# Kernel optimization log

Measured on AMD Instinct MI355X. Metric: run time of the kernel, lower is better.

Reference implementation:

```python
import jax, jax.numpy as jnp
import numpy as np

B, C, H, W = 16, 64, 64, 64
K = 512  # n_embeddings


def setup_inputs() -> dict:
    key = jax.random.key(0)
    k1, k2 = jax.random.split(key)
    inputs = jax.random.normal(k1, (B, C, H, W), dtype=jnp.float32)
    emb_weight = jax.random.normal(k2, (K, C), dtype=jnp.float32)
    weight = jnp.ones((K,), dtype=jnp.float32)  # EMA cluster-size buffer
    return {"inputs": inputs, "emb_weight": emb_weight, "weight": weight}


def reference(inputs, emb_weight, weight):
    sg = jax.lax.stop_gradient
    # BCHW -> BHWC
    x = jnp.transpose(inputs, (0, 2, 3, 1))  # [B,H,W,C]
    flat = x.reshape(-1, x.shape[-1])        # [N,C]
    n = flat.shape[0]
    k = emb_weight.shape[0]
    # squared euclidean distances [N,K] (argmin identical to cdist argmin)
    d = (
        jnp.sum(flat * flat, axis=-1, keepdims=True)
        - 2.0 * (flat @ emb_weight.T)
        + jnp.sum(emb_weight * emb_weight, axis=-1)
    )
    indices = jnp.argmin(d, axis=1)  # [N]
    # avg_probs = mean over rows of one-hot mask == normalized histogram
    avg_probs = jnp.bincount(indices, length=k).astype(jnp.float32) / jnp.float32(n)
    perplexity = jnp.exp(-jnp.sum(avg_probs * jnp.log(avg_probs + 1e-10)))
    # straight-through quantization
    q = emb_weight[indices].reshape(x.shape)  # [B,H,W,C]
    quantized = sg(q) + x - sg(x)
    commitment_loss = jnp.mean((sg(quantized) - x) ** 2)
    active_codes = jnp.sum(weight >= 0.01)
    out = jnp.transpose(quantized, (0, 3, 1, 2))  # back to BCHW
    return out, commitment_loss, perplexity, active_codes, indices
```

## Files before the change

kernel.cpp:

```cpp
#include <hip/hip_runtime.h>

#define HW 4096
#define CHW 262144
#define OUT_ELEMS 4194304
#define FLT_BIG 3.4e38f

typedef __attribute__((ext_vector_type(8))) short  short8;
typedef __attribute__((ext_vector_type(4))) float  floatx4;
typedef __attribute__((ext_vector_type(4))) int    intx4;


__device__ __forceinline__ unsigned bf16_rne(float f) {
    unsigned u = __float_as_uint(f);
    return (u + 0x7FFFu + ((u >> 16) & 1u)) >> 16;
}

__device__ __forceinline__ void split8(const float* f, intx4* hi, intx4* lo) {
    unsigned h[4], l[4];
#pragma unroll
    for (int j = 0; j < 4; ++j) {
        const unsigned h0 = bf16_rne(f[2 * j]);
        const unsigned h1 = bf16_rne(f[2 * j + 1]);
        const float hf0 = __uint_as_float(h0 << 16);
        const float hf1 = __uint_as_float(h1 << 16);
        const unsigned l0 = bf16_rne(f[2 * j] - hf0);
        const unsigned l1 = bf16_rne(f[2 * j + 1] - hf1);
        h[j] = h0 | (h1 << 16);
        l[j] = l0 | (l1 << 16);
    }
    *hi = intx4{(int)h[0], (int)h[1], (int)h[2], (int)h[3]};
    *lo = intx4{(int)l[0], (int)l[1], (int)l[2], (int)l[3]};
}

__global__ void vq_prep(const float* __restrict__ emb,
                        unsigned short* __restrict__ pfrag,
                        float* __restrict__ enorm) {
    const int t = threadIdx.x;
    const int lane = t & 63;
#pragma unroll
    for (int i = 0; i < 8; ++i) {
        const int f    = (i << 8) + t;
        const int code = (blockIdx.x << 5) + (f >> 6);
        const int c    = lane;
        const float v  = emb[(code << 6) + c];
        const unsigned hb = bf16_rne(v);
        const float hf    = __uint_as_float(hb << 16);
        const unsigned lb = bf16_rne(v - hf);
        const int nc = code >> 6, grp = (code & 63) >> 4, n = code & 15;
        const int q = (c & 31) >> 3, o = c & 7;
        const int jh = c >> 5;
        const int jl = 2 + (c >> 5);
        pfrag[((((size_t)(nc*4 + jh)*4 + grp)*4 + q)*16 + n)*8 + o] = (unsigned short)hb;
        pfrag[((((size_t)(nc*4 + jl)*4 + grp)*4 + q)*16 + n)*8 + o] = (unsigned short)lb;
        float s = v * v;
#pragma unroll
        for (int off = 32; off > 0; off >>= 1) s += __shfl_xor(s, off, 64);
        if (lane == 0) enorm[code] = s;
    }
}

__global__ __launch_bounds__(256)
void vq_main(const float* __restrict__ x_in, const float* __restrict__ emb,
             const unsigned short* __restrict__ pfrag,
             const float* __restrict__ enorm,
             float* __restrict__ out, float* __restrict__ idx_out,
             double* __restrict__ ws_sse) {
    __shared__ float  b1s[2][32], b2s[2][32];
    __shared__ int    i1s[2][32], i2s[2][32];
    __shared__ int    c1i[32], c2i[32], qidx[32];
    __shared__ double parts[8][32];
    __shared__ double ls_red[4];

    const int t     = threadIdx.x;
    const int lane  = t & 63;
    const int wv    = t >> 6;
    const int col   = lane & 15;
    const int quad  = lane >> 4;
    const int blk   = blockIdx.x;
    const int mrow0 = (wv >> 1) << 4;
    const int khalf = wv & 1;
    const int ncol0 = khalf << 5;
    const int half = blk & 1;
    const int bh = blk >> 1;
    const int b = bh >> 6, h = bh & 63;
    const float* xb = x_in + (size_t)b * CHW + h * 64 + (half << 5);

    short8 Ah[2], Al[2];
#pragma unroll
    for (int u = 0; u < 2; ++u) {
        float f[8];
#pragma unroll
        for (int j = 0; j < 8; ++j) {
            const int c = (u << 5) + (quad << 3) + j;
            f[j] = xb[(size_t)c * HW + mrow0 + col];
        }
        intx4 hi, lo;
        split8(f, &hi, &lo);
        Ah[u] = __builtin_bit_cast(short8, hi);
        Al[u] = __builtin_bit_cast(short8, lo);
    }

    float B1[4], B2[4]; int I1[4], I2[4];
#pragma unroll
    for (int s = 0; s < 4; ++s) { B1[s] = FLT_BIG; B2[s] = FLT_BIG; I1[s] = 0x3FFFFFFF; I2[s] = 0x3FFFFFFF; }

    const char* pf = (const char*)pfrag + (size_t)lane * 16 + ((size_t)khalf << 11);

#pragma unroll 2
    for (int nc = 0; nc < 8; ++nc) {
        const char* base = pf + ((size_t)nc << 14);
        const int K0 = nc << 6;
        const float en0 = enorm[K0 + ncol0 + col];
        const float en1 = enorm[K0 + ncol0 + 16 + col];

        floatx4 a0{0.f,0.f,0.f,0.f}, a1{0.f,0.f,0.f,0.f};
#define BLD(j, g) (*(const short8*)(base + ((j) << 12) + ((g) << 10)))
        {
            const short8 b0 = BLD(0, 0), b1 = BLD(0, 1);
            a0 = __builtin_amdgcn_mfma_f32_16x16x32_bf16(Ah[0], b0, a0, 0, 0, 0);
            a1 = __builtin_amdgcn_mfma_f32_16x16x32_bf16(Ah[0], b1, a1, 0, 0, 0);
            a0 = __builtin_amdgcn_mfma_f32_16x16x32_bf16(Al[0], b0, a0, 0, 0, 0);
            a1 = __builtin_amdgcn_mfma_f32_16x16x32_bf16(Al[0], b1, a1, 0, 0, 0);
        }
        {
            const short8 b0 = BLD(1, 0), b1 = BLD(1, 1);
            a0 = __builtin_amdgcn_mfma_f32_16x16x32_bf16(Ah[1], b0, a0, 0, 0, 0);
            a1 = __builtin_amdgcn_mfma_f32_16x16x32_bf16(Ah[1], b1, a1, 0, 0, 0);
            a0 = __builtin_amdgcn_mfma_f32_16x16x32_bf16(Al[1], b0, a0, 0, 0, 0);
            a1 = __builtin_amdgcn_mfma_f32_16x16x32_bf16(Al[1], b1, a1, 0, 0, 0);
        }
        {
            const short8 b0 = BLD(2, 0), b1 = BLD(2, 1);
            a0 = __builtin_amdgcn_mfma_f32_16x16x32_bf16(Ah[0], b0, a0, 0, 0, 0);
            a1 = __builtin_amdgcn_mfma_f32_16x16x32_bf16(Ah[0], b1, a1, 0, 0, 0);
        }
        {
            const short8 b0 = BLD(3, 0), b1 = BLD(3, 1);
            a0 = __builtin_amdgcn_mfma_f32_16x16x32_bf16(Ah[1], b0, a0, 0, 0, 0);
            a1 = __builtin_amdgcn_mfma_f32_16x16x32_bf16(Ah[1], b1, a1, 0, 0, 0);
        }
#undef BLD

#pragma unroll
        for (int nt = 0; nt < 2; ++nt) {
            const int code = K0 + ncol0 + (nt << 4) + col;
            const float en = nt ? en1 : en0;
            const floatx4 av = nt ? a1 : a0;
#pragma unroll
            for (int reg = 0; reg < 4; ++reg) {
                const float d = fmaf(-2.f, av[reg], en);
                if (d < B1[reg])      { B2[reg] = B1[reg]; I2[reg] = I1[reg]; B1[reg] = d; I1[reg] = code; }
                else if (d < B2[reg]) { B2[reg] = d; I2[reg] = code; }
            }
        }
    }

#pragma unroll
    for (int off = 1; off <= 8; off <<= 1) {
#pragma unroll
        for (int s = 0; s < 4; ++s) {
            const float ob1 = __shfl_xor(B1[s], off, 64);
            const int   oi1 = __shfl_xor(I1[s], off, 64);
            const float ob2 = __shfl_xor(B2[s], off, 64);
            const int   oi2 = __shfl_xor(I2[s], off, 64);
            if (ob1 < B1[s] || (ob1 == B1[s] && oi1 < I1[s])) {
                float nb2; int ni2;
                if (B1[s] < ob2 || (B1[s] == ob2 && I1[s] < oi2)) { nb2 = B1[s]; ni2 = I1[s]; }
                else                                              { nb2 = ob2;  ni2 = oi2; }
                B1[s] = ob1; I1[s] = oi1; B2[s] = nb2; I2[s] = ni2;
            } else if (ob1 < B2[s] || (ob1 == B2[s] && oi1 < I2[s])) {
                B2[s] = ob1; I2[s] = oi1;
            }
        }
    }
    if (col == 0) {
#pragma unroll
        for (int s = 0; s < 4; ++s) {
            const int row = mrow0 + (quad << 2) + s;
            b1s[khalf][row] = B1[s]; b2s[khalf][row] = B2[s];
            i1s[khalf][row] = I1[s]; i2s[khalf][row] = I2[s];
        }
    }
    __syncthreads();

    if (t < 32) {
        const int r = t;
        float b1 = b1s[0][r], b2 = b2s[0][r];
        int   i1 = i1s[0][r], i2 = i2s[0][r];
        const float c1 = b1s[1][r]; const int j1 = i1s[1][r];
        const float c2 = b2s[1][r]; const int j2 = i2s[1][r];
        if (c1 < b1 || (c1 == b1 && j1 < i1))      { b2 = b1; i2 = i1; b1 = c1; i1 = j1; }
        else if (c1 < b2 || (c1 == b2 && j1 < i2)) { b2 = c1; i2 = j1; }
        if (c2 < b2 || (c2 == b2 && j2 < i2))      { b2 = c2; i2 = j2; }
        c1i[r] = i1; c2i[r] = i2;
    }
    __syncthreads();

    {
        const int r  = t & 31;
        const int k  = t >> 5;
        const int cq = k >> 1;
        const int code = (k & 1) ? c2i[r] : c1i[r];
        const float* ep = emb + ((size_t)code << 6) + (cq << 4);
        const float* xq = xb + r;
        double d0 = 0.0, d1 = 0.0;
#pragma unroll
        for (int cc = 0; cc < 16; cc += 2) {
            const int c = (cq << 4) + cc;
            const double f0 = (double)xq[(size_t)c * HW]       - (double)ep[cc];
            const double f1 = (double)xq[(size_t)(c + 1) * HW] - (double)ep[cc + 1];
            d0 = fma(f0, f0, d0);
            d1 = fma(f1, f1, d1);
        }
        parts[k][r] = d0 + d1;
    }
    __syncthreads();
    if (t < 32) {
        const double d1 = parts[0][t] + parts[2][t] + parts[4][t] + parts[6][t];
        const double d2 = parts[1][t] + parts[3][t] + parts[5][t] + parts[7][t];
        int i1 = c1i[t];
        const int i2 = c2i[t];
        if (d2 < d1 || (d2 == d1 && i2 < i1)) i1 = i2;
        qidx[t] = i1;
        idx_out[(blk << 5) + t] = (float)i1;
    }
    __syncthreads();

    {
        const int r  = t & 31;
        const int c0 = (t >> 5) << 3;
        const float* xp = xb + r;
        float*       op = out + (size_t)b * CHW + h * 64 + (half << 5) + r;
        const float* eq = emb + ((size_t)qidx[r] << 6);
        float sse_local = 0.f;
#pragma unroll
        for (int cc = 0; cc < 8; ++cc) {
            const int c = c0 + cc;
            const float qc = eq[c];
            const float dx = qc - xp[(size_t)c * HW];
            sse_local = fmaf(dx, dx, sse_local);
            op[(size_t)c * HW] = qc;
        }
#pragma unroll
        for (int off = 32; off > 0; off >>= 1)
            sse_local += __shfl_down(sse_local, off, 64);
        if (lane == 0) ls_red[wv] = (double)sse_local;
        __syncthreads();
        if (t == 0)
            ws_sse[blk] = (ls_red[0] + ls_red[1]) + (ls_red[2] + ls_red[3]);
    }
}

__global__ void vq_hist(const float* __restrict__ idx_out,
                        unsigned* __restrict__ part) {
    __shared__ unsigned hs[512];
    const int t = threadIdx.x;
    hs[t] = 0u; hs[t + 256] = 0u;
    __syncthreads();
    const float4* ip = (const float4*)(idx_out + (blockIdx.x << 12));
#pragma unroll
    for (int i = 0; i < 4; ++i) {
        const float4 v = ip[(i << 8) + t];
        atomicAdd(&hs[(int)v.x], 1u);
        atomicAdd(&hs[(int)v.y], 1u);
        atomicAdd(&hs[(int)v.z], 1u);
        atomicAdd(&hs[(int)v.w], 1u);
    }
    __syncthreads();
    unsigned* pp = part + (blockIdx.x << 9);
    pp[t] = hs[t]; pp[t + 256] = hs[t + 256];
}

__global__ void vq_scal(const unsigned* __restrict__ part,
                        const double* __restrict__ ws_sse,
                        const float* __restrict__ weight,
                        float* __restrict__ scal) {
    __shared__ double redt[8], reds[8];
    __shared__ int    redi[8];
    const int k = threadIdx.x;
    const int lane = k & 63, wv = k >> 6;
    unsigned cnt = 0;
#pragma unroll
    for (int p = 0; p < 16; ++p) cnt += part[(p << 9) + k];
    const double pr = (double)cnt / 65536.0;
    double term = pr * log(pr + 1e-10);
    double ssep = 0.0;
#pragma unroll
    for (int j = 0; j < 4; ++j) ssep += ws_sse[k + (j << 9)];
    int act = (weight[k] >= 0.01f) ? 1 : 0;
#pragma unroll
    for (int off = 32; off > 0; off >>= 1) {
        term += __shfl_down(term, off, 64);
        ssep += __shfl_down(ssep, off, 64);
        act  += __shfl_down(act,  off, 64);
    }
    if (lane == 0) { redt[wv] = term; reds[wv] = ssep; redi[wv] = act; }
    __syncthreads();
    if (k == 0) {
        double s = 0.0, ss = 0.0; int a = 0;
#pragma unroll
        for (int i = 0; i < 8; ++i) { s += redt[i]; ss += reds[i]; a += redi[i]; }
        scal[0] = (float)(ss / 4194304.0);
        scal[1] = (float)exp(-s);
        scal[2] = (float)a;
    }
}

extern "C" void kernel_launch(void* const* d_in, const int* in_sizes, int n_in,
                              void* d_out, int out_size, void* d_ws, size_t ws_size,
                              hipStream_t stream) {
    const float* x      = (const float*)d_in[0];
    const float* emb    = (const float*)d_in[1];
    const float* weight = (const float*)d_in[2];

    float* out = (float*)d_out;
    float*          enorm  = (float*)d_ws;
    unsigned short* pfrag  = (unsigned short*)((char*)d_ws + 4096);
    double*         ws_sse = (double*)((char*)d_ws + 135168);
    unsigned*       part   = (unsigned*)((char*)d_ws + 151552);

    float* scal    = out + OUT_ELEMS;
    float* idx_out = out + OUT_ELEMS + 3;

    vq_prep<<<16, 256, 0, stream>>>(emb, pfrag, enorm);
    vq_main<<<2048, 256, 0, stream>>>(x, emb, pfrag, enorm, out, idx_out, ws_sse);
    vq_hist<<<16, 256, 0, stream>>>(idx_out, part);
    vq_scal<<<1, 512, 0, stream>>>(part, ws_sse, weight, scal);
}
```

Before: 121.8 us.

## Fuse histogram and scalar reduction into main kernel via last-block pattern

Removes the separate histogram and scalar kernels. vq_main now atomically updates a global histogram and striped SSE accumulators, and the last block to finish computes perplexity, loss and active-code count. The MFMA operands are swapped so codes lie along rows, which lets each lane track the best two candidates for a single point and needs fewer shuffle steps. The -0.5*||e||^2 term is folded into the accumulator initialisation, turning the search into an argmax. vq_prep also uses more blocks and zeroes the counters. This cuts two launches, but global atomics and the last-block fence pattern add contention and ordering risk.

```diff
diff --git a/kernel.cpp b/kernel.cpp
--- a/kernel.cpp
+++ b/kernel.cpp
@@ -34,42 +34,50 @@
 
 __global__ void vq_prep(const float* __restrict__ emb,
                         unsigned short* __restrict__ pfrag,
-                        float* __restrict__ enorm) {
+                        float* __restrict__ enorm,
+                        unsigned* __restrict__ hist,
+                        unsigned* __restrict__ done,
+                        double* __restrict__ ssep) {
     const int t = threadIdx.x;
     const int lane = t & 63;
-#pragma unroll
-    for (int i = 0; i < 8; ++i) {
-        const int f    = (i << 8) + t;
-        const int code = (blockIdx.x << 5) + (f >> 6);
-        const int c    = lane;
-        const float v  = emb[(code << 6) + c];
-        const unsigned hb = bf16_rne(v);
-        const float hf    = __uint_as_float(hb << 16);
-        const unsigned lb = bf16_rne(v - hf);
-        const int nc = code >> 6, grp = (code & 63) >> 4, n = code & 15;
-        const int q = (c & 31) >> 3, o = c & 7;
-        const int jh = c >> 5;
-        const int jl = 2 + (c >> 5);
-        pfrag[((((size_t)(nc*4 + jh)*4 + grp)*4 + q)*16 + n)*8 + o] = (unsigned short)hb;
-        pfrag[((((size_t)(nc*4 + jl)*4 + grp)*4 + q)*16 + n)*8 + o] = (unsigned short)lb;
-        float s = v * v;
-#pragma unroll
-        for (int off = 32; off > 0; off >>= 1) s += __shfl_xor(s, off, 64);
-        if (lane == 0) enorm[code] = s;
-    }
+    if (blockIdx.x == 0) {
+        hist[t] = 0u; hist[t + 256] = 0u;
+        if (t == 0) *done = 0u;
+        if (t < 32) ssep[t] = 0.0;
+    }
+    const int code = (blockIdx.x << 2) + (t >> 6);
+    const int c = lane;
+    const float v = emb[(code << 6) + c];
+    const unsigned hb = bf16_rne(v);
+    const float hf    = __uint_as_float(hb << 16);
+    const unsigned lb = bf16_rne(v - hf);
+    const int nc = code >> 6, grp = (code & 63) >> 4, n = code & 15;
+    const int q = (c & 31) >> 3, o = c & 7;
+    const int jh = c >> 5;
+    const int jl = 2 + (c >> 5);
+    pfrag[((((size_t)(nc*4 + jh)*4 + grp)*4 + q)*16 + n)*8 + o] = (unsigned short)hb;
+    pfrag[((((size_t)(nc*4 + jl)*4 + grp)*4 + q)*16 + n)*8 + o] = (unsigned short)lb;
+    float s = v * v;
+#pragma unroll
+    for (int off = 32; off > 0; off >>= 1) s += __shfl_xor(s, off, 64);
+    if (lane == 0) enorm[code] = -0.5f * s;
 }
 
 __global__ __launch_bounds__(256)
 void vq_main(const float* __restrict__ x_in, const float* __restrict__ emb,
              const unsigned short* __restrict__ pfrag,
              const float* __restrict__ enorm,
+             const float* __restrict__ weight,
              float* __restrict__ out, float* __restrict__ idx_out,
-             double* __restrict__ ws_sse) {
+             float* __restrict__ scal,
+             unsigned* __restrict__ hist, unsigned* __restrict__ done,
+             double* __restrict__ ssep) {
     __shared__ float  b1s[2][32], b2s[2][32];
     __shared__ int    i1s[2][32], i2s[2][32];
     __shared__ int    c1i[32], c2i[32], qidx[32];
     __shared__ double parts[8][32];
     __shared__ double ls_red[4];
+    __shared__ int    lastf;
 
     const int t     = threadIdx.x;
     const int lane  = t & 63;
@@ -85,7 +93,7 @@
     const int b = bh >> 6, h = bh & 63;
     const float* xb = x_in + (size_t)b * CHW + h * 64 + (half << 5);
 
-    short8 Ah[2], Al[2];
+    short8 Xh[2], Xl[2];
 #pragma unroll
     for (int u = 0; u < 2; ++u) {
         float f[8];
@@ -96,90 +104,91 @@
         }
         intx4 hi, lo;
         split8(f, &hi, &lo);
-        Ah[u] = __builtin_bit_cast(short8, hi);
-        Al[u] = __builtin_bit_cast(short8, lo);
-    }
-
-    float B1[4], B2[4]; int I1[4], I2[4];
-#pragma unroll
-    for (int s = 0; s < 4; ++s) { B1[s] = FLT_BIG; B2[s] = FLT_BIG; I1[s] = 0x3FFFFFFF; I2[s] = 0x3FFFFFFF; }
-
-    const char* pf = (const char*)pfrag + (size_t)lane * 16 + ((size_t)khalf << 11);
+        Xh[u] = __builtin_bit_cast(short8, hi);
+        Xl[u] = __builtin_bit_cast(short8, lo);
+    }
+
+    float B1a = -FLT_BIG, B2a = -FLT_BIG, B1b = -FLT_BIG, B2b = -FLT_BIG;
+    int   I1a = 0x3FFFFFFF, I2a = 0x3FFFFFFF, I1b = 0x3FFFFFFF, I2b = 0x3FFFFFFF;
+
+    const char*  pf  = (const char*)pfrag + (size_t)lane * 16 + ((size_t)khalf << 11);
+    const float* enp = enorm + ncol0 + (quad << 2);
 
 #pragma unroll 2
     for (int nc = 0; nc < 8; ++nc) {
         const char* base = pf + ((size_t)nc << 14);
         const int K0 = nc << 6;
-        const float en0 = enorm[K0 + ncol0 + col];
-        const float en1 = enorm[K0 + ncol0 + 16 + col];
-
-        floatx4 a0{0.f,0.f,0.f,0.f}, a1{0.f,0.f,0.f,0.f};
+        floatx4 a0 = *(const floatx4*)(enp + K0);
+        floatx4 a1 = *(const floatx4*)(enp + K0 + 16);
 #define BLD(j, g) (*(const short8*)(base + ((j) << 12) + ((g) << 10)))
         {
-            const short8 b0 = BLD(0, 0), b1 = BLD(0, 1);
-            a0 = __builtin_amdgcn_mfma_f32_16x16x32_bf16(Ah[0], b0, a0, 0, 0, 0);
-            a1 = __builtin_amdgcn_mfma_f32_16x16x32_bf16(Ah[0], b1, a1, 0, 0, 0);
-            a0 = __builtin_amdgcn_mfma_f32_16x16x32_bf16(Al[0], b0, a0, 0, 0, 0);
-            a1 = __builtin_amdgcn_mfma_f32_16x16x32_bf16(Al[0], b1, a1, 0, 0, 0);
+            const short8 e0 = BLD(0, 0), e1 = BLD(0, 1);
+            a0 = __builtin_amdgcn_mfma_f32_16x16x32_bf16(e0, Xh[0], a0, 0, 0, 0);
+            a1 = __builtin_amdgcn_mfma_f32_16x16x32_bf16(e1, Xh[0], a1, 0, 0, 0);
+            a0 = __builtin_amdgcn_mfma_f32_16x16x32_bf16(e0, Xl[0], a0, 0, 0, 0);
+            a1 = __builtin_amdgcn_mfma_f32_16x16x32_bf16(e1, Xl[0], a1, 0, 0, 0);
         }
         {
-            const short8 b0 = BLD(1, 0), b1 = BLD(1, 1);
-            a0 = __builtin_amdgcn_mfma_f32_16x16x32_bf16(Ah[1], b0, a0, 0, 0, 0);
-            a1 = __builtin_amdgcn_mfma_f32_16x16x32_bf16(Ah[1], b1, a1, 0, 0, 0);
-            a0 = __builtin_amdgcn_mfma_f32_16x16x32_bf16(Al[1], b0, a0, 0, 0, 0);
-            a1 = __builtin_amdgcn_mfma_f32_16x16x32_bf16(Al[1], b1, a1, 0, 0, 0);
+            const short8 e0 = BLD(1, 0), e1 = BLD(1, 1);
+            a0 = __builtin_amdgcn_mfma_f32_16x16x32_bf16(e0, Xh[1], a0, 0, 0, 0);
+            a1 = __builtin_amdgcn_mfma_f32_16x16x32_bf16(e1, Xh[1], a1, 0, 0, 0);
+            a0 = __builtin_amdgcn_mfma_f32_16x16x32_bf16(e0, Xl[1], a0, 0, 0, 0);
+            a1 = __builtin_amdgcn_mfma_f32_16x16x32_bf16(e1, Xl[1], a1, 0, 0, 0);
         }
         {
-            const short8 b0 = BLD(2, 0), b1 = BLD(2, 1);
-            a0 = __builtin_amdgcn_mfma_f32_16x16x32_bf16(Ah[0], b0, a0, 0, 0, 0);
-            a1 = __builtin_amdgcn_mfma_f32_16x16x32_bf16(Ah[0], b1, a1, 0, 0, 0);
+            const short8 e0 = BLD(2, 0), e1 = BLD(2, 1);
+            a0 = __builtin_amdgcn_mfma_f32_16x16x32_bf16(e0, Xh[0], a0, 0, 0, 0);
+            a1 = __builtin_amdgcn_mfma_f32_16x16x32_bf16(e1, Xh[0], a1, 0, 0, 0);
         }
         {
-            const short8 b0 = BLD(3, 0), b1 = BLD(3, 1);
-            a0 = __builtin_amdgcn_mfma_f32_16x16x32_bf16(Ah[1], b0, a0, 0, 0, 0);
-            a1 = __builtin_amdgcn_mfma_f32_16x16x32_bf16(Ah[1], b1, a1, 0, 0, 0);
+            const short8 e0 = BLD(3, 0), e1 = BLD(3, 1);
+            a0 = __builtin_amdgcn_mfma_f32_16x16x32_bf16(e0, Xh[1], a0, 0, 0, 0);
+            a1 = __builtin_amdgcn_mfma_f32_16x16x32_bf16(e1, Xh[1], a1, 0, 0, 0);
         }
 #undef BLD
 
-#pragma unroll
-        for (int nt = 0; nt < 2; ++nt) {
-            const int code = K0 + ncol0 + (nt << 4) + col;
-            const float en = nt ? en1 : en0;
-            const floatx4 av = nt ? a1 : a0;
-#pragma unroll
-            for (int reg = 0; reg < 4; ++reg) {
-                const float d = fmaf(-2.f, av[reg], en);
-                if (d < B1[reg])      { B2[reg] = B1[reg]; I2[reg] = I1[reg]; B1[reg] = d; I1[reg] = code; }
-                else if (d < B2[reg]) { B2[reg] = d; I2[reg] = code; }
-            }
-        }
-    }
-
-#pragma unroll
-    for (int off = 1; off <= 8; off <<= 1) {
-#pragma unroll
-        for (int s = 0; s < 4; ++s) {
-            const float ob1 = __shfl_xor(B1[s], off, 64);
-            const int   oi1 = __shfl_xor(I1[s], off, 64);
-            const float ob2 = __shfl_xor(B2[s], off, 64);
-            const int   oi2 = __shfl_xor(I2[s], off, 64);
-            if (ob1 < B1[s] || (ob1 == B1[s] && oi1 < I1[s])) {
-                float nb2; int ni2;
-                if (B1[s] < ob2 || (B1[s] == ob2 && I1[s] < oi2)) { nb2 = B1[s]; ni2 = I1[s]; }
-                else                                              { nb2 = ob2;  ni2 = oi2; }
-                B1[s] = ob1; I1[s] = oi1; B2[s] = nb2; I2[s] = ni2;
-            } else if (ob1 < B2[s] || (ob1 == B2[s] && oi1 < I2[s])) {
-                B2[s] = ob1; I2[s] = oi1;
-            }
-        }
-    }
-    if (col == 0) {
-#pragma unroll
-        for (int s = 0; s < 4; ++s) {
-            const int row = mrow0 + (quad << 2) + s;
-            b1s[khalf][row] = B1[s]; b2s[khalf][row] = B2[s];
-            i1s[khalf][row] = I1[s]; i2s[khalf][row] = I2[s];
-        }
+        const int cb = K0 + ncol0 + (quad << 2);
+#pragma unroll
+        for (int reg = 0; reg < 4; ++reg) {
+            const float da = a0[reg];
+            if (da > B1a)      { B2a = B1a; I2a = I1a; B1a = da; I1a = cb + reg; }
+            else if (da > B2a) { B2a = da; I2a = cb + reg; }
+            const float db = a1[reg];
+            if (db > B1b)      { B2b = B1b; I2b = I1b; B1b = db; I1b = cb + 16 + reg; }
+            else if (db > B2b) { B2b = db; I2b = cb + 16 + reg; }
+        }
+    }
+
+    float B1, B2; int I1, I2;
+    if (B1b > B1a || (B1b == B1a && I1b < I1a)) {
+        B1 = B1b; I1 = I1b;
+        if (B1a > B2b || (B1a == B2b && I1a < I2b)) { B2 = B1a; I2 = I1a; }
+        else                                        { B2 = B2b; I2 = I2b; }
+    } else {
+        B1 = B1a; I1 = I1a;
+        if (B1b > B2a || (B1b == B2a && I1b < I2a)) { B2 = B1b; I2 = I1b; }
+        else                                        { B2 = B2a; I2 = I2a; }
+    }
+
+#pragma unroll
+    for (int off = 16; off <= 32; off <<= 1) {
+        const float ob1 = __shfl_xor(B1, off, 64);
+        const int   oi1 = __shfl_xor(I1, off, 64);
+        const float ob2 = __shfl_xor(B2, off, 64);
+        const int   oi2 = __shfl_xor(I2, off, 64);
+        if (ob1 > B1 || (ob1 == B1 && oi1 < I1)) {
+            float nb2; int ni2;
+            if (B1 > ob2 || (B1 == ob2 && I1 < oi2)) { nb2 = B1; ni2 = I1; }
+            else                                     { nb2 = ob2; ni2 = oi2; }
+            B1 = ob1; I1 = oi1; B2 = nb2; I2 = ni2;
+        } else if (ob1 > B2 || (ob1 == B2 && oi1 < I2)) {
+            B2 = ob1; I2 = oi1;
+        }
+    }
+    if (lane < 16) {
+        const int row = mrow0 + lane;
+        b1s[khalf][row] = B1; b2s[khalf][row] = B2;
+        i1s[khalf][row] = I1; i2s[khalf][row] = I2;
     }
     __syncthreads();
 
@@ -189,9 +198,9 @@
         int   i1 = i1s[0][r], i2 = i2s[0][r];
         const float c1 = b1s[1][r]; const int j1 = i1s[1][r];
         const float c2 = b2s[1][r]; const int j2 = i2s[1][r];
-        if (c1 < b1 || (c1 == b1 && j1 < i1))      { b2 = b1; i2 = i1; b1 = c1; i1 = j1; }
-        else if (c1 < b2 || (c1 == b2 && j1 < i2)) { b2 = c1; i2 = j1; }
-        if (c2 < b2 || (c2 == b2 && j2 < i2))      { b2 = c2; i2 = j2; }
+        if (c1 > b1 || (c1 == b1 && j1 < i1))      { b2 = b1; i2 = i1; b1 = c1; i1 = j1; }
+        else if (c1 > b2 || (c1 == b2 && j1 < i2)) { b2 = c1; i2 = j1; }
+        if (c2 > b2 || (c2 == b2 && j2 < i2))      { b2 = c2; i2 = j2; }
         c1i[r] = i1; c2i[r] = i2;
     }
     __syncthreads();
@@ -223,6 +232,7 @@
         if (d2 < d1 || (d2 == d1 && i2 < i1)) i1 = i2;
         qidx[t] = i1;
         idx_out[(blk << 5) + t] = (float)i1;
+        atomicAdd(&hist[i1], 1u);
     }
     __syncthreads();
 
@@ -247,62 +257,45 @@
         if (lane == 0) ls_red[wv] = (double)sse_local;
         __syncthreads();
         if (t == 0)
-            ws_sse[blk] = (ls_red[0] + ls_red[1]) + (ls_red[2] + ls_red[3]);
-    }
-}
-
-__global__ void vq_hist(const float* __restrict__ idx_out,
-                        unsigned* __restrict__ part) {
-    __shared__ unsigned hs[512];
-    const int t = threadIdx.x;
-    hs[t] = 0u; hs[t + 256] = 0u;
-    __syncthreads();
-    const float4* ip = (const float4*)(idx_out + (blockIdx.x << 12));
-#pragma unroll
-    for (int i = 0; i < 4; ++i) {
-        const float4 v = ip[(i << 8) + t];
-        atomicAdd(&hs[(int)v.x], 1u);
-        atomicAdd(&hs[(int)v.y], 1u);
-        atomicAdd(&hs[(int)v.z], 1u);
-        atomicAdd(&hs[(int)v.w], 1u);
-    }
-    __syncthreads();
-    unsigned* pp = part + (blockIdx.x << 9);
-    pp[t] = hs[t]; pp[t + 256] = hs[t + 256];
-}
-
-__global__ void vq_scal(const unsigned* __restrict__ part,
-                        const double* __restrict__ ws_sse,
-                        const float* __restrict__ weight,
-                        float* __restrict__ scal) {
-    __shared__ double redt[8], reds[8];
-    __shared__ int    redi[8];
-    const int k = threadIdx.x;
-    const int lane = k & 63, wv = k >> 6;
-    unsigned cnt = 0;
-#pragma unroll
-    for (int p = 0; p < 16; ++p) cnt += part[(p << 9) + k];
-    const double pr = (double)cnt / 65536.0;
-    double term = pr * log(pr + 1e-10);
-    double ssep = 0.0;
-#pragma unroll
-    for (int j = 0; j < 4; ++j) ssep += ws_sse[k + (j << 9)];
-    int act = (weight[k] >= 0.01f) ? 1 : 0;
-#pragma unroll
-    for (int off = 32; off > 0; off >>= 1) {
-        term += __shfl_down(term, off, 64);
-        ssep += __shfl_down(ssep, off, 64);
-        act  += __shfl_down(act,  off, 64);
-    }
-    if (lane == 0) { redt[wv] = term; reds[wv] = ssep; redi[wv] = act; }
-    __syncthreads();
-    if (k == 0) {
-        double s = 0.0, ss = 0.0; int a = 0;
-#pragma unroll
-        for (int i = 0; i < 8; ++i) { s += redt[i]; ss += reds[i]; a += redi[i]; }
-        scal[0] = (float)(ss / 4194304.0);
-        scal[1] = (float)exp(-s);
-        scal[2] = (float)a;
+            atomicAdd(&ssep[blk & 31],
+                      (ls_red[0] + ls_red[1]) + (ls_red[2] + ls_red[3]));
+    }
+
+    if (t == 0) {
+        __threadfence();
+        lastf = (atomicAdd(done, 1u) == 2047u) ? 1 : 0;
+    }
+    __syncthreads();
+    if (lastf) {
+        __threadfence();
+        double term = 0.0; int act = 0;
+#pragma unroll
+        for (int j = 0; j < 2; ++j) {
+            const int k = t + (j << 8);
+            const unsigned cnt =
+                __hip_atomic_load(&hist[k], __ATOMIC_RELAXED, __HIP_MEMORY_SCOPE_AGENT);
+            const double pr = (double)cnt * (1.0 / 65536.0);
+            term += pr * log(pr + 1e-10);
+            act  += (weight[k] >= 0.01f) ? 1 : 0;
+        }
+#pragma unroll
+        for (int off = 32; off > 0; off >>= 1) {
+            term += __shfl_down(term, off, 64);
+            act  += __shfl_down(act,  off, 64);
+        }
+        if (lane == 0) { ls_red[wv] = term; c1i[wv] = act; }
+        __syncthreads();
+        if (t == 0) {
+            const double s = (ls_red[0] + ls_red[1]) + (ls_red[2] + ls_red[3]);
+            const int    a = c1i[0] + c1i[1] + c1i[2] + c1i[3];
+            double ss = 0.0;
+#pragma unroll
+            for (int p = 0; p < 32; ++p)
+                ss += __hip_atomic_load(&ssep[p], __ATOMIC_RELAXED, __HIP_MEMORY_SCOPE_AGENT);
+            scal[0] = (float)(ss * (1.0 / 4194304.0));
+            scal[1] = (float)exp(-s);
+            scal[2] = (float)a;
+        }
     }
 }
 
@@ -314,16 +307,16 @@
     const float* weight = (const float*)d_in[2];
 
     float* out = (float*)d_out;
-    float*          enorm  = (float*)d_ws;
-    unsigned short* pfrag  = (unsigned short*)((char*)d_ws + 4096);
-    double*         ws_sse = (double*)((char*)d_ws + 135168);
-    unsigned*       part   = (unsigned*)((char*)d_ws + 151552);
+    float*          enorm = (float*)d_ws;
+    unsigned short* pfrag = (unsigned short*)((char*)d_ws + 4096);
+    double*         ssep  = (double*)((char*)d_ws + 135168);
+    unsigned*       hist  = (unsigned*)((char*)d_ws + 135424);
+    unsigned*       done  = (unsigned*)((char*)d_ws + 137472);
 
     float* scal    = out + OUT_ELEMS;
     float* idx_out = out + OUT_ELEMS + 3;
 
-    vq_prep<<<16, 256, 0, stream>>>(emb, pfrag, enorm);
-    vq_main<<<2048, 256, 0, stream>>>(x, emb, pfrag, enorm, out, idx_out, ws_sse);
-    vq_hist<<<16, 256, 0, stream>>>(idx_out, part);
-    vq_scal<<<1, 512, 0, stream>>>(part, ws_sse, weight, scal);
-}
+    vq_prep<<<128, 256, 0, stream>>>(emb, pfrag, enorm, hist, done, ssep);
+    vq_main<<<2048, 256, 0, stream>>>(x, emb, pfrag, enorm, weight,
+                                      out, idx_out, scal, hist, done, ssep);
+}
```

Result: slower. 173.0 us (+42.0%).
